# Kernel optimization log

Measured on AMD Instinct MI355X. Metric: run time of the kernel, lower is better.

The kernel has to match this reference:

```python
import jax, jax.numpy as jnp
import numpy as np

B, L, H, E = 4, 2048, 8, 64
S, D = L, E  # causal mask forces L == S


def setup_inputs() -> dict:
    key = jax.random.key(0)
    kq, kk, kv, km = jax.random.split(key, 4)
    return {
        "queries": jax.random.normal(kq, (B, L, H, E), dtype=jnp.float32),
        "keys": jax.random.normal(kk, (B, S, H, E), dtype=jnp.float32),
        "values": jax.random.normal(kv, (B, S, H, D), dtype=jnp.float32),
        "map": jax.random.normal(km, (S, S), dtype=jnp.float32),
    }


def reference(queries, keys, values, map):
    # queries: [B,L,H,E], keys: [B,S,H,E], values: [B,S,H,D], map: [S,S]
    E_ = queries.shape[-1]
    scale = 1.0 / jnp.sqrt(jnp.asarray(E_, dtype=queries.dtype))
    # raw attention scores: [B,H,L,S]
    scores = jnp.einsum("blhe,bshe->bhls", queries, keys)
    # mix scores with learned map along the key axis: [B,H,L,S]
    scores = jnp.einsum("bhls,st->bhlt", scores, map)
    # causal mask (TriangularCausalMask: triu with diagonal=1 is masked)
    Lq = queries.shape[1]
    causal = jnp.triu(jnp.ones((Lq, Lq), dtype=bool), k=1)  # [L,S]
    scores = jnp.where(causal[None, None, :, :], -jnp.inf, scores)
    attn = jax.nn.softmax(scale * scores, axis=-1)  # dropout p=0.0 -> identity
    out = jnp.einsum("bhls,bshd->blhd", attn, values)  # [B,L,H,D]
    return out
```

## Files before the change

### kernel.cpp

```cpp
#include <hip/hip_runtime.h>


typedef short bf16x8 __attribute__((ext_vector_type(8)));
typedef float f32x4 __attribute__((ext_vector_type(4)));
typedef float f32x16 __attribute__((ext_vector_type(16)));
typedef unsigned short u16x8 __attribute__((ext_vector_type(8)));
typedef unsigned int u32x4 __attribute__((ext_vector_type(4)));

typedef __attribute__((address_space(1))) const void gvoid;
typedef __attribute__((address_space(3))) void lvoid;

__device__ __forceinline__ unsigned short f2bf(float x) {
  unsigned int u = __float_as_uint(x);
  u += 0x7FFFu + ((u >> 16) & 1u);
  return (unsigned short)(u >> 16);
}
__device__ __forceinline__ float bf2f(unsigned short h) {
  return __uint_as_float(((unsigned int)h) << 16);
}
__device__ __forceinline__ unsigned int cvtpk(float lo, float hi) {
  unsigned int r;
  asm("v_cvt_pk_bf16_f32 %0, %1, %2" : "=v"(r) : "v"(lo), "v"(hi));
  return r;
}

__device__ __forceinline__ void gload16(const unsigned short* g, unsigned short* l) {
  __builtin_amdgcn_global_load_lds((gvoid*)g, (lvoid*)l, 16, 0, 0);
}

template <int NW>
__device__ __forceinline__ void stage_tile(const unsigned short* __restrict__ g,
                                           int gstride, unsigned short* l,
                                           int rows, int tid) {
  const int lane = tid & 63, w = tid >> 6;
  const int nch = rows << 3;
  for (int c0 = (w << 6); c0 < nch; c0 += NW * 64) {
    const int c = c0 + lane;
    const int row = c >> 3;
    const int bir = (c & 7) << 4;
    const int sb = bir ^ ((row & 7) << 4);
    gload16(g + (size_t)row * gstride + (sb >> 1), l + (size_t)c0 * 8);
  }
}

__device__ __forceinline__ int swz(int row, int byteInRow) {
  return row * 128 + (byteInRow ^ ((row & 7) << 4));
}

__global__ __launch_bounds__(256) void prep_all(
    const float* __restrict__ M, const float* __restrict__ K,
    const float* __restrict__ V, unsigned short* __restrict__ Mth,
    unsigned short* __restrict__ Mtl, unsigned short* __restrict__ Kth,
    unsigned short* __restrict__ Ktl, unsigned short* __restrict__ Vts) {
  __shared__ float Ts[64][68];
  const int s0 = blockIdx.x << 6;
  const int role = (int)blockIdx.y >> 5;
  const int yy = (int)blockIdx.y & 31;
  const int tid = threadIdx.x, r = tid >> 2, c0 = (tid & 3) << 4;

  const float* src;
  if (role == 0) {
    src = M + (size_t)(s0 + r) * 2048 + (yy << 6) + c0;
  } else {
    const int b = yy >> 3, h = yy & 7;
    const float* base = (role == 1) ? K : V;
    src = base + ((size_t)(b * 2048 + s0 + r) * 8 + h) * 64 + c0;
  }
#pragma unroll
  for (int j = 0; j < 4; ++j)
    *(float4*)&Ts[r][c0 + 4 * j] = *(const float4*)(src + 4 * j);
  __syncthreads();

  u16x8 h0, h1, l0v, l1v;
#pragma unroll
  for (int j = 0; j < 8; ++j) {
    float x = Ts[c0 + j][r];
    unsigned short hh = f2bf(x);
    h0[j] = hh; l0v[j] = f2bf(x - bf2f(hh));
  }
#pragma unroll
  for (int j = 8; j < 16; ++j) {
    float x = Ts[c0 + j][r];
    unsigned short hh = f2bf(x);
    h1[j - 8] = hh; l1v[j - 8] = f2bf(x - bf2f(hh));
  }

  if (role == 0) {
    const size_t o = (size_t)((yy << 6) + r) * 2048 + s0 + c0;
    *(u16x8*)(Mth + o) = h0; *(u16x8*)(Mth + o + 8) = h1;
    *(u16x8*)(Mtl + o) = l0v; *(u16x8*)(Mtl + o + 8) = l1v;
  } else {
    const size_t o = ((size_t)yy * 64 + r) * 2048 + s0 + c0;
    if (role == 1) {
      *(u16x8*)(Kth + o) = h0; *(u16x8*)(Kth + o + 8) = h1;
      *(u16x8*)(Ktl + o) = l0v; *(u16x8*)(Ktl + o + 8) = l1v;
    } else {
      *(u16x8*)(Vts + o) = h0; *(u16x8*)(Vts + o + 8) = h1;
    }
  }
}

__global__ __launch_bounds__(256) void km_mfma(
    const unsigned short* __restrict__ Mth, const unsigned short* __restrict__ Mtl,
    const unsigned short* __restrict__ Kth, const unsigned short* __restrict__ Ktl,
    unsigned short* __restrict__ KMh, unsigned short* __restrict__ KMl) {
  __shared__ __attribute__((aligned(16))) unsigned short sm[24576];
  unsigned short* MtH = sm;
  unsigned short* MtL = sm + 8192;
  unsigned short* KtH = sm + 16384;
  unsigned short* KtL = sm + 20480;
  const int tid = threadIdx.x, lane = tid & 63, w = tid >> 6;
  const int g = lane >> 4, li = lane & 15;
  const int t0 = blockIdx.x << 7;
  const int bh = blockIdx.y;
  const unsigned short* KtHb = Kth + (size_t)bh * 64 * 2048;
  const unsigned short* KtLb = Ktl + (size_t)bh * 64 * 2048;

  f32x4 acc[2][4];
#pragma unroll
  for (int mi = 0; mi < 2; ++mi)
#pragma unroll
    for (int ni = 0; ni < 4; ++ni) acc[mi][ni] = (f32x4){0.f, 0.f, 0.f, 0.f};

  for (int s0 = 0; s0 < 2048; s0 += 64) {
    __syncthreads();
    stage_tile<4>(Mth + (size_t)t0 * 2048 + s0, 2048, MtH, 128, tid);
    stage_tile<4>(Mtl + (size_t)t0 * 2048 + s0, 2048, MtL, 128, tid);
    stage_tile<4>(KtHb + s0, 2048, KtH, 64, tid);
    stage_tile<4>(KtLb + s0, 2048, KtL, 64, tid);
    asm volatile("s_waitcnt vmcnt(0)" ::: "memory");
    __syncthreads();
#pragma unroll
    for (int kk = 0; kk < 2; ++kk) {
      const int kb = (kk * 32 + 8 * g) * 2;
      bf16x8 aH[2], aL[2];
#pragma unroll
      for (int mi = 0; mi < 2; ++mi) {
        const int row = (w << 5) + (mi << 4) + li;
        aH[mi] = *(const bf16x8*)((const char*)MtH + swz(row, kb));
        aL[mi] = *(const bf16x8*)((const char*)MtL + swz(row, kb));
      }
#pragma unroll
      for (int ni = 0; ni < 4; ++ni) {
        const int row = (ni << 4) + li;
        const int off = swz(row, kb);
        const bf16x8 bH = *(const bf16x8*)((const char*)KtH + off);
        const bf16x8 bL = *(const bf16x8*)((const char*)KtL + off);
#pragma unroll
        for (int mi = 0; mi < 2; ++mi) {
          acc[mi][ni] = __builtin_amdgcn_mfma_f32_16x16x32_bf16(aH[mi], bH, acc[mi][ni], 0, 0, 0);
          acc[mi][ni] = __builtin_amdgcn_mfma_f32_16x16x32_bf16(aH[mi], bL, acc[mi][ni], 0, 0, 0);
          acc[mi][ni] = __builtin_amdgcn_mfma_f32_16x16x32_bf16(aL[mi], bH, acc[mi][ni], 0, 0, 0);
        }
      }
    }
  }
  const size_t base = (size_t)bh * 2048 * 64;
#pragma unroll
  for (int mi = 0; mi < 2; ++mi)
#pragma unroll
    for (int r = 0; r < 4; ++r) {
      const int trow = t0 + (w << 5) + (mi << 4) + (g << 2) + r;
#pragma unroll
      for (int ni = 0; ni < 4; ++ni) {
        const float x = acc[mi][ni][r];
        const unsigned short hh = f2bf(x);
        const size_t idx = base + (size_t)trow * 64 + (ni << 4) + li;
        KMh[idx] = hh;
        KMl[idx] = f2bf(x - bf2f(hh));
      }
    }
}

__global__ __launch_bounds__(256, 3) void attn32(
    const float* __restrict__ Q, const unsigned short* __restrict__ KMh,
    const unsigned short* __restrict__ KMl, const unsigned short* __restrict__ Vt,
    float* __restrict__ Out, unsigned short* __restrict__ Opart,
    float* __restrict__ Ml) {
  __shared__ __attribute__((aligned(16))) unsigned short sm[24576];
  const int tid = threadIdx.x, lane = tid & 63, w = tid >> 6;
  const int g2 = lane >> 5, li5 = lane & 31;

  const int bid = (int)blockIdx.x;
  const int x = bid & 7, n = bid >> 3;
  const int slot = n >> 5, j = n & 31;
  const int bh = (x << 2) | (j & 3);
  const int kk = j >> 2;
  int lt, jt0, jtEnd;
  bool partial;
  if (slot == 2) {
    lt = kk; jt0 = 0; jtEnd = 2 * kk + 1; partial = false;
  } else {
    lt = 15 - kk;
    const int half = 16 - kk;
    jt0 = slot * half; jtEnd = jt0 + half - 1; partial = true;
  }
  const int b = bh >> 3, h = bh & 7;
  const int l0 = lt << 7;
  const int qg = l0 + (w << 5) + li5;
  const int rloc = (w << 5) + li5;

  const float SC2 = 0.18033688011112042f;
  bf16x8 qh[4], ql[4];
  {
    const float* qsrc = Q + (((size_t)(b * 2048 + qg) * 8 + h) << 6) + (g2 << 3);
#pragma unroll
    for (int kki = 0; kki < 4; ++kki) {
      const float4 v0 = *(const float4*)(qsrc + 16 * kki);
      const float4 v1 = *(const float4*)(qsrc + 16 * kki + 4);
      const float xs[8] = {v0.x, v0.y, v0.z, v0.w, v1.x, v1.y, v1.z, v1.w};
#pragma unroll
      for (int jj = 0; jj < 8; ++jj) {
        const float xv = xs[jj] * SC2;
        const unsigned short hh = f2bf(xv);
        qh[kki][jj] = (short)hh;
        ql[kki][jj] = (short)f2bf(xv - bf2f(hh));
      }
    }
  }

  f32x16 o0 = {0,0,0,0,0,0,0,0,0,0,0,0,0,0,0,0};
  f32x16 o1 = {0,0,0,0,0,0,0,0,0,0,0,0,0,0,0,0};
  f32x16 lsacc = {0,0,0,0,0,0,0,0,0,0,0,0,0,0,0,0};
  float m2 = -1e30f;
  bf16x8 ones;
#pragma unroll
  for (int jj = 0; jj < 8; ++jj) ones[jj] = (short)0x3F80;

  const unsigned short* KHb = KMh + (size_t)bh * 2048 * 64;
  const unsigned short* KLb = KMl + (size_t)bh * 2048 * 64;
  const unsigned short* VTb = Vt + (size_t)bh * 64 * 2048;

  const int jtmax_w = 2 * lt + (w >> 1);

  {
    unsigned short* s0b = sm + (jt0 & 1) * 12288;
    stage_tile<4>(KHb + (size_t)jt0 * 4096, 64, s0b, 64, tid);
    stage_tile<4>(KLb + (size_t)jt0 * 4096, 64, s0b + 4096, 64, tid);
    stage_tile<4>(VTb + jt0 * 64, 2048, s0b + 8192, 64, tid);
  }
  asm volatile("s_waitcnt vmcnt(0)" ::: "memory");
  __builtin_amdgcn_s_barrier();
  __builtin_amdgcn_sched_barrier(0);

  for (int jt = jt0; jt <= jtEnd; ++jt) {
    const int cur = jt & 1;
    if (jt < jtEnd) {
      unsigned short* nb = sm + (cur ^ 1) * 12288;
      stage_tile<4>(KHb + (size_t)(jt + 1) * 4096, 64, nb, 64, tid);
      stage_tile<4>(KLb + (size_t)(jt + 1) * 4096, 64, nb + 4096, 64, tid);
      stage_tile<4>(VTb + (jt + 1) * 64, 2048, nb + 8192, 64, tid);
    }

    if (jt <= jtmax_w) {
      const unsigned short* KH = sm + cur * 12288;
      const unsigned short* KL = KH + 4096;
      const unsigned short* VT = KH + 8192;

      f32x16 z0 = {0,0,0,0,0,0,0,0,0,0,0,0,0,0,0,0};
      f32x16 z1 = {0,0,0,0,0,0,0,0,0,0,0,0,0,0,0,0};
      __builtin_amdgcn_s_setprio(1);
#pragma unroll
      for (int kki = 0; kki < 4; ++kki) {
        const int cb = 32 * kki + 16 * g2;
        const bf16x8 a0h = *(const bf16x8*)((const char*)KH + swz(li5, cb));
        const bf16x8 a0l = *(const bf16x8*)((const char*)KL + swz(li5, cb));
        const bf16x8 a1h = *(const bf16x8*)((const char*)KH + swz(32 + li5, cb));
        const bf16x8 a1l = *(const bf16x8*)((const char*)KL + swz(32 + li5, cb));
        z0 = __builtin_amdgcn_mfma_f32_32x32x16_bf16(a0h, qh[kki], z0, 0, 0, 0);
        z0 = __builtin_amdgcn_mfma_f32_32x32x16_bf16(a0h, ql[kki], z0, 0, 0, 0);
        z0 = __builtin_amdgcn_mfma_f32_32x32x16_bf16(a0l, qh[kki], z0, 0, 0, 0);
        z1 = __builtin_amdgcn_mfma_f32_32x32x16_bf16(a1h, qh[kki], z1, 0, 0, 0);
        z1 = __builtin_amdgcn_mfma_f32_32x32x16_bf16(a1h, ql[kki], z1, 0, 0, 0);
        z1 = __builtin_amdgcn_mfma_f32_32x32x16_bf16(a1l, qh[kki], z1, 0, 0, 0);
      }
      __builtin_amdgcn_s_setprio(0);

      const bool needmask = (jt * 64 + 63 > l0 + (w << 5));
      if (needmask) {
        const int thr = qg - jt * 64;
#pragma unroll
        for (int rr = 0; rr < 16; ++rr) {
          const int tl = (g2 << 2) + ((rr >> 2) << 3) + (rr & 3);
          if (tl > thr) z0[rr] = -1e30f;
          if (tl + 32 > thr) z1[rr] = -1e30f;
        }
      }

      float t16[16];
#pragma unroll
      for (int rr = 0; rr < 16; ++rr) t16[rr] = fmaxf(z0[rr], z1[rr]);
#pragma unroll
      for (int s = 8; s; s >>= 1)
#pragma unroll
        for (int rr = 0; rr < 8; ++rr)
          if (rr < s) t16[rr] = fmaxf(t16[rr], t16[rr + s]);
      const float mx = fmaxf(t16[0], __shfl_xor(t16[0], 32));
      if (__any(mx > m2 + 11.0f)) {
        const float m2n = fmaxf(m2, mx);
        const float fs = exp2f(m2 - m2n);
        m2 = m2n;
#pragma unroll
        for (int rr = 0; rr < 16; ++rr) { o0[rr] *= fs; o1[rr] *= fs; }
        lsacc[0] *= fs;
      }

      float pv0[16], pv1[16];
#pragma unroll
      for (int rr = 0; rr < 16; ++rr) {
        pv0[rr] = exp2f(z0[rr] - m2);
        pv1[rr] = exp2f(z1[rr] - m2);
      }
      unsigned int W0[8], W1[8];
#pragma unroll
      for (int i = 0; i < 8; ++i) {
        W0[i] = cvtpk(pv0[2 * i], pv0[2 * i + 1]);
        W1[i] = cvtpk(pv1[2 * i], pv1[2 * i + 1]);
      }
      asm volatile("v_permlane32_swap_b32 %0, %1" : "+v"(W0[0]), "+v"(W0[2]));
      asm volatile("v_permlane32_swap_b32 %0, %1" : "+v"(W0[1]), "+v"(W0[3]));
      asm volatile("v_permlane32_swap_b32 %0, %1" : "+v"(W0[4]), "+v"(W0[6]));
      asm volatile("v_permlane32_swap_b32 %0, %1" : "+v"(W0[5]), "+v"(W0[7]));
      asm volatile("v_permlane32_swap_b32 %0, %1" : "+v"(W1[0]), "+v"(W1[2]));
      asm volatile("v_permlane32_swap_b32 %0, %1" : "+v"(W1[1]), "+v"(W1[3]));
      asm volatile("v_permlane32_swap_b32 %0, %1" : "+v"(W1[4]), "+v"(W1[6]));
      asm volatile("v_permlane32_swap_b32 %0, %1" : "+v"(W1[5]), "+v"(W1[7]));
      bf16x8 pf[4];
      {
        u32x4 f0 = {W0[0], W0[1], W0[2], W0[3]};
        u32x4 f1 = {W0[4], W0[5], W0[6], W0[7]};
        u32x4 f2 = {W1[0], W1[1], W1[2], W1[3]};
        u32x4 f3 = {W1[4], W1[5], W1[6], W1[7]};
        pf[0] = __builtin_bit_cast(bf16x8, f0);
        pf[1] = __builtin_bit_cast(bf16x8, f1);
        pf[2] = __builtin_bit_cast(bf16x8, f2);
        pf[3] = __builtin_bit_cast(bf16x8, f3);
      }

      __builtin_amdgcn_s_setprio(1);
#pragma unroll
      for (int kki = 0; kki < 4; ++kki) {
        const int cb = 32 * kki + 16 * g2;
        const bf16x8 v0f = *(const bf16x8*)((const char*)VT + swz(li5, cb));
        const bf16x8 v1f = *(const bf16x8*)((const char*)VT + swz(32 + li5, cb));
        o0 = __builtin_amdgcn_mfma_f32_32x32x16_bf16(v0f, pf[kki], o0, 0, 0, 0);
        o1 = __builtin_amdgcn_mfma_f32_32x32x16_bf16(v1f, pf[kki], o1, 0, 0, 0);
        lsacc = __builtin_amdgcn_mfma_f32_32x32x16_bf16(ones, pf[kki], lsacc, 0, 0, 0);
      }
      __builtin_amdgcn_s_setprio(0);
    }

    asm volatile("s_waitcnt vmcnt(0)" ::: "memory");
    __builtin_amdgcn_s_barrier();
    __builtin_amdgcn_sched_barrier(0);
  }

  if (!partial) {
    const float inv = 1.f / lsacc[0];
    float* ob = Out + (((size_t)(b * 2048 + qg) * 8 + h) << 6);
#pragma unroll
    for (int r2 = 0; r2 < 4; ++r2) {
      const int doff = (g2 << 2) + (r2 << 3);
      float4 s0 = make_float4(o0[4 * r2] * inv, o0[4 * r2 + 1] * inv,
                              o0[4 * r2 + 2] * inv, o0[4 * r2 + 3] * inv);
      *(float4*)(ob + doff) = s0;
      float4 s1 = make_float4(o1[4 * r2] * inv, o1[4 * r2 + 1] * inv,
                              o1[4 * r2 + 2] * inv, o1[4 * r2 + 3] * inv);
      *(float4*)(ob + 32 + doff) = s1;
    }
  } else {
    const size_t pidx = ((size_t)bh * 8 + kk) * 128 + rloc;
    unsigned short* op = Opart + (size_t)slot * 2097152 + pidx * 64;
#pragma unroll
    for (int r2 = 0; r2 < 4; ++r2) {
      const int doff = (g2 << 2) + (r2 << 3);
      uint2 pa, pb;
      pa.x = cvtpk(o0[4 * r2], o0[4 * r2 + 1]);
      pa.y = cvtpk(o0[4 * r2 + 2], o0[4 * r2 + 3]);
      *(uint2*)(op + doff) = pa;
      pb.x = cvtpk(o1[4 * r2], o1[4 * r2 + 1]);
      pb.y = cvtpk(o1[4 * r2 + 2], o1[4 * r2 + 3]);
      *(uint2*)(op + 32 + doff) = pb;
    }
    float* mlp = Ml + ((size_t)slot * 32768 + pidx) * 2;
    mlp[0] = m2;
    mlp[1] = lsacc[0];
  }
}

__global__ __launch_bounds__(256) void attn_combine(
    const unsigned short* __restrict__ Opart, const float* __restrict__ Ml,
    float* __restrict__ Out) {
  const int tid = threadIdx.x;
  const int rowg = (int)blockIdx.x * 32 + (tid >> 3);
  const int d0 = (tid & 7) << 3;
  const int r = rowg & 127, kk = (rowg >> 7) & 7, bh = rowg >> 10;
  const int b = bh >> 3, h = bh & 7;
  const int lt = 15 - kk;
  const size_t pidx = (((size_t)bh * 8 + kk) * 128 + r);
  const size_t HOFF = 2097152;
  const size_t MOFF = 65536;
  const float m0 = Ml[pidx * 2], ls0 = Ml[pidx * 2 + 1];
  const float m1 = Ml[MOFF + pidx * 2], ls1 = Ml[MOFF + pidx * 2 + 1];
  const float mm = fmaxf(m0, m1);
  const float w0 = exp2f(m0 - mm), w1 = exp2f(m1 - mm);
  const float inv = 1.f / (ls0 * w0 + ls1 * w1);
  const u16x8 A = *(const u16x8*)(Opart + pidx * 64 + d0);
  const u16x8 Bv = *(const u16x8*)(Opart + HOFF + pidx * 64 + d0);
  float res[8];
#pragma unroll
  for (int jj = 0; jj < 8; ++jj)
    res[jj] = (bf2f(A[jj]) * w0 + bf2f(Bv[jj]) * w1) * inv;
  const int qg = lt * 128 + r;
  float* o = Out + (((size_t)(b * 2048 + qg) * 8 + h) << 6) + d0;
  *(float4*)o = make_float4(res[0], res[1], res[2], res[3]);
  *(float4*)(o + 4) = make_float4(res[4], res[5], res[6], res[7]);
}

extern "C" void kernel_launch(void* const* d_in, const int* in_sizes, int n_in,
                              void* d_out, int out_size, void* d_ws, size_t ws_size,
                              hipStream_t stream) {
  const float* Q = (const float*)d_in[0];
  const float* K = (const float*)d_in[1];
  const float* V = (const float*)d_in[2];
  const float* M = (const float*)d_in[3];
  float* Out = (float*)d_out;
  char* ws = (char*)d_ws;
  const size_t MB = 1u << 20;
  unsigned short* Mth = (unsigned short*)(ws);
  unsigned short* Mtl = (unsigned short*)(ws + 8 * MB);
  unsigned short* Kth = (unsigned short*)(ws + 16 * MB);
  unsigned short* Ktl = (unsigned short*)(ws + 24 * MB);
  unsigned short* Vts = (unsigned short*)(ws + 32 * MB);
  unsigned short* KMh = (unsigned short*)(ws + 40 * MB);
  unsigned short* KMl = (unsigned short*)(ws + 48 * MB);
  unsigned short* Opart = (unsigned short*)(ws);
  float* Mlp = (float*)(ws + 8 * MB);

  prep_all<<<dim3(32, 96), 256, 0, stream>>>(M, K, V, Mth, Mtl, Kth, Ktl, Vts);
  km_mfma<<<dim3(16, 32), 256, 0, stream>>>(Mth, Mtl, Kth, Ktl, KMh, KMl);
  attn32<<<dim3(768), 256, 0, stream>>>(Q, KMh, KMl, Vts, Out, Opart, Mlp);
  attn_combine<<<dim3(1024), 256, 0, stream>>>(Opart, Mlp, Out);
}
```

Baseline: 139.1 us.

## Rewrite K·map GEMM with 32x32 MFMA and split-K across waves

The km_mfma kernel switches from 16x16x32 to 32x32x16 bf16 MFMA tiles. Waves are split into two row groups and two K-halves, and the partial sums are reduced through shared memory before the hi/lo bf16 output is written. It also raises wave priority around the MFMA block. The aim is fewer LDS fragment loads per MFMA and better matrix-core efficiency, at the cost of an extra LDS reduction pass and only half the waves doing the final stores.

```diff
diff --git a/kernel.cpp b/kernel.cpp
--- a/kernel.cpp
+++ b/kernel.cpp
@@ -100,7 +100,7 @@
   }
 }
 
-__global__ __launch_bounds__(256) void km_mfma(
+__global__ __launch_bounds__(256) void km_mfma32(
     const unsigned short* __restrict__ Mth, const unsigned short* __restrict__ Mtl,
     const unsigned short* __restrict__ Kth, const unsigned short* __restrict__ Ktl,
     unsigned short* __restrict__ KMh, unsigned short* __restrict__ KMl) {
@@ -110,17 +110,19 @@
   unsigned short* KtH = sm + 16384;
   unsigned short* KtL = sm + 20480;
   const int tid = threadIdx.x, lane = tid & 63, w = tid >> 6;
-  const int g = lane >> 4, li = lane & 15;
+  const int g2 = lane >> 5, li5 = lane & 31;
+  const int tg = w & 1, ks = w >> 1;
   const int t0 = blockIdx.x << 7;
   const int bh = blockIdx.y;
   const unsigned short* KtHb = Kth + (size_t)bh * 64 * 2048;
   const unsigned short* KtLb = Ktl + (size_t)bh * 64 * 2048;
 
-  f32x4 acc[2][4];
-#pragma unroll
-  for (int mi = 0; mi < 2; ++mi)
-#pragma unroll
-    for (int ni = 0; ni < 4; ++ni) acc[mi][ni] = (f32x4){0.f, 0.f, 0.f, 0.f};
+  f32x16 acc[2][2];
+#pragma unroll
+  for (int tf = 0; tf < 2; ++tf)
+#pragma unroll
+    for (int ef = 0; ef < 2; ++ef)
+      acc[tf][ef] = (f32x16){0,0,0,0,0,0,0,0,0,0,0,0,0,0,0,0};
 
   for (int s0 = 0; s0 < 2048; s0 += 64) {
     __syncthreads();
@@ -130,46 +132,71 @@
     stage_tile<4>(KtLb + s0, 2048, KtL, 64, tid);
     asm volatile("s_waitcnt vmcnt(0)" ::: "memory");
     __syncthreads();
-#pragma unroll
-    for (int kk = 0; kk < 2; ++kk) {
-      const int kb = (kk * 32 + 8 * g) * 2;
-      bf16x8 aH[2], aL[2];
-#pragma unroll
-      for (int mi = 0; mi < 2; ++mi) {
-        const int row = (w << 5) + (mi << 4) + li;
-        aH[mi] = *(const bf16x8*)((const char*)MtH + swz(row, kb));
-        aL[mi] = *(const bf16x8*)((const char*)MtL + swz(row, kb));
-      }
-#pragma unroll
-      for (int ni = 0; ni < 4; ++ni) {
-        const int row = (ni << 4) + li;
-        const int off = swz(row, kb);
-        const bf16x8 bH = *(const bf16x8*)((const char*)KtH + off);
-        const bf16x8 bL = *(const bf16x8*)((const char*)KtL + off);
-#pragma unroll
-        for (int mi = 0; mi < 2; ++mi) {
-          acc[mi][ni] = __builtin_amdgcn_mfma_f32_16x16x32_bf16(aH[mi], bH, acc[mi][ni], 0, 0, 0);
-          acc[mi][ni] = __builtin_amdgcn_mfma_f32_16x16x32_bf16(aH[mi], bL, acc[mi][ni], 0, 0, 0);
-          acc[mi][ni] = __builtin_amdgcn_mfma_f32_16x16x32_bf16(aL[mi], bH, acc[mi][ni], 0, 0, 0);
+
+    __builtin_amdgcn_s_setprio(1);
+#pragma unroll
+    for (int kgi = 0; kgi < 2; ++kgi) {
+      const int kb = ((ks << 1) + kgi) * 32 + (g2 << 4);
+      const int ra0 = (tg << 6) + li5;
+      const bf16x8 aH0 = *(const bf16x8*)((const char*)MtH + swz(ra0, kb));
+      const bf16x8 aL0 = *(const bf16x8*)((const char*)MtL + swz(ra0, kb));
+      const bf16x8 aH1 = *(const bf16x8*)((const char*)MtH + swz(ra0 + 32, kb));
+      const bf16x8 aL1 = *(const bf16x8*)((const char*)MtL + swz(ra0 + 32, kb));
+      const bf16x8 bH0 = *(const bf16x8*)((const char*)KtH + swz(li5, kb));
+      const bf16x8 bL0 = *(const bf16x8*)((const char*)KtL + swz(li5, kb));
+      const bf16x8 bH1 = *(const bf16x8*)((const char*)KtH + swz(32 + li5, kb));
+      const bf16x8 bL1 = *(const bf16x8*)((const char*)KtL + swz(32 + li5, kb));
+      acc[0][0] = __builtin_amdgcn_mfma_f32_32x32x16_bf16(aH0, bH0, acc[0][0], 0, 0, 0);
+      acc[0][0] = __builtin_amdgcn_mfma_f32_32x32x16_bf16(aH0, bL0, acc[0][0], 0, 0, 0);
+      acc[0][0] = __builtin_amdgcn_mfma_f32_32x32x16_bf16(aL0, bH0, acc[0][0], 0, 0, 0);
+      acc[0][1] = __builtin_amdgcn_mfma_f32_32x32x16_bf16(aH0, bH1, acc[0][1], 0, 0, 0);
+      acc[0][1] = __builtin_amdgcn_mfma_f32_32x32x16_bf16(aH0, bL1, acc[0][1], 0, 0, 0);
+      acc[0][1] = __builtin_amdgcn_mfma_f32_32x32x16_bf16(aL0, bH1, acc[0][1], 0, 0, 0);
+      acc[1][0] = __builtin_amdgcn_mfma_f32_32x32x16_bf16(aH1, bH0, acc[1][0], 0, 0, 0);
+      acc[1][0] = __builtin_amdgcn_mfma_f32_32x32x16_bf16(aH1, bL0, acc[1][0], 0, 0, 0);
+      acc[1][0] = __builtin_amdgcn_mfma_f32_32x32x16_bf16(aL1, bH0, acc[1][0], 0, 0, 0);
+      acc[1][1] = __builtin_amdgcn_mfma_f32_32x32x16_bf16(aH1, bH1, acc[1][1], 0, 0, 0);
+      acc[1][1] = __builtin_amdgcn_mfma_f32_32x32x16_bf16(aH1, bL1, acc[1][1], 0, 0, 0);
+      acc[1][1] = __builtin_amdgcn_mfma_f32_32x32x16_bf16(aL1, bH1, acc[1][1], 0, 0, 0);
+    }
+    __builtin_amdgcn_s_setprio(0);
+  }
+
+  __syncthreads();
+  float* red = (float*)sm;
+  if (ks == 1) {
+#pragma unroll
+    for (int tf = 0; tf < 2; ++tf)
+#pragma unroll
+      for (int ef = 0; ef < 2; ++ef) {
+        const int fi = (tg << 2) | (tf << 1) | ef;
+        float* dst = red + (size_t)(fi * 64 + lane) * 17;
+#pragma unroll
+        for (int rr = 0; rr < 16; ++rr) dst[rr] = acc[tf][ef][rr];
+      }
+  }
+  __syncthreads();
+  if (ks == 0) {
+    const size_t base = (size_t)bh * (2048 * 64);
+#pragma unroll
+    for (int tf = 0; tf < 2; ++tf)
+#pragma unroll
+      for (int ef = 0; ef < 2; ++ef) {
+        const int fi = (tg << 2) | (tf << 1) | ef;
+        const float* src = red + (size_t)(fi * 64 + lane) * 17;
+#pragma unroll
+        for (int rr = 0; rr < 16; ++rr) {
+          const float v = acc[tf][ef][rr] + src[rr];
+          const int trow = t0 + (tg << 6) + (tf << 5) + (g2 << 2) +
+                           ((rr >> 2) << 3) + (rr & 3);
+          const int e = (ef << 5) + li5;
+          const unsigned short hh = f2bf(v);
+          const size_t idx = base + (size_t)trow * 64 + e;
+          KMh[idx] = hh;
+          KMl[idx] = f2bf(v - bf2f(hh));
         }
       }
-    }
-  }
-  const size_t base = (size_t)bh * 2048 * 64;
-#pragma unroll
-  for (int mi = 0; mi < 2; ++mi)
-#pragma unroll
-    for (int r = 0; r < 4; ++r) {
-      const int trow = t0 + (w << 5) + (mi << 4) + (g << 2) + r;
-#pragma unroll
-      for (int ni = 0; ni < 4; ++ni) {
-        const float x = acc[mi][ni][r];
-        const unsigned short hh = f2bf(x);
-        const size_t idx = base + (size_t)trow * 64 + (ni << 4) + li;
-        KMh[idx] = hh;
-        KMl[idx] = f2bf(x - bf2f(hh));
-      }
-    }
+  }
 }
 
 __global__ __launch_bounds__(256, 3) void attn32(
@@ -438,7 +465,7 @@
   float* Mlp = (float*)(ws + 8 * MB);
 
   prep_all<<<dim3(32, 96), 256, 0, stream>>>(M, K, V, Mth, Mtl, Kth, Ktl, Vts);
-  km_mfma<<<dim3(16, 32), 256, 0, stream>>>(Mth, Mtl, Kth, Ktl, KMh, KMl);
+  km_mfma32<<<dim3(16, 32), 256, 0, stream>>>(Mth, Mtl, Kth, Ktl, KMh, KMl);
   attn32<<<dim3(768), 256, 0, stream>>>(Q, KMh, KMl, Vts, Out, Opart, Mlp);
   attn_combine<<<dim3(1024), 256, 0, stream>>>(Opart, Mlp, Out);
 }
```

After: 147.8 us. +6.3%, slower.
